# Performance work log

Measured on AMD Instinct MI355X. Metric: run time of the kernel, lower is better.

The kernel has to match this reference:

```python
import jax, jax.numpy as jnp
import numpy as np

HID = 10


def _lstm_cell(xt, h, c, W_ih, W_hh, b_ih, b_hh):
    # PyTorch LSTMCell: gates ordered (i, f, g, o)
    gates = xt @ W_ih.T + b_ih + h @ W_hh.T + b_hh  # [B, 4*HID]
    i, f, g, o = jnp.split(gates, 4, axis=-1)
    c_new = jax.nn.sigmoid(f) * c + jax.nn.sigmoid(i) * jnp.tanh(g)
    h_new = jax.nn.sigmoid(o) * jnp.tanh(c_new)
    return h_new, c_new


def setup_inputs() -> dict:
    key = jax.random.key(0)
    ks = jax.random.split(key, 12)
    B, T = 2048, 1024
    s = 0.1
    return {
        "x": jax.random.normal(ks[0], (B, T), dtype=jnp.float32),
        "W_ih1": jax.random.normal(ks[1], (4 * HID, 1), dtype=jnp.float32) * s,
        "W_hh1": jax.random.normal(ks[2], (4 * HID, HID), dtype=jnp.float32) * s,
        "b_ih1": jax.random.normal(ks[3], (4 * HID,), dtype=jnp.float32) * s,
        "b_hh1": jax.random.normal(ks[4], (4 * HID,), dtype=jnp.float32) * s,
        "W_ih2": jax.random.normal(ks[5], (4 * HID, HID), dtype=jnp.float32) * s,
        "W_hh2": jax.random.normal(ks[6], (4 * HID, HID), dtype=jnp.float32) * s,
        "b_ih2": jax.random.normal(ks[7], (4 * HID,), dtype=jnp.float32) * s,
        "b_ih2b": None,  # placeholder removed below
        "b_hh2": jax.random.normal(ks[8], (4 * HID,), dtype=jnp.float32) * s,
        "W_lin": jax.random.normal(ks[9], (1, HID), dtype=jnp.float32) * s,
        "b_lin": jax.random.normal(ks[10], (1,), dtype=jnp.float32) * s,
        "future": 64,
    } if False else {
        "x": jax.random.normal(ks[0], (B, T), dtype=jnp.float32),
        "W_ih1": jax.random.normal(ks[1], (4 * HID, 1), dtype=jnp.float32) * s,
        "W_hh1": jax.random.normal(ks[2], (4 * HID, HID), dtype=jnp.float32) * s,
        "b_ih1": jax.random.normal(ks[3], (4 * HID,), dtype=jnp.float32) * s,
        "b_hh1": jax.random.normal(ks[4], (4 * HID,), dtype=jnp.float32) * s,
        "W_ih2": jax.random.normal(ks[5], (4 * HID, HID), dtype=jnp.float32) * s,
        "W_hh2": jax.random.normal(ks[6], (4 * HID, HID), dtype=jnp.float32) * s,
        "b_ih2": jax.random.normal(ks[7], (4 * HID,), dtype=jnp.float32) * s,
        "b_hh2": jax.random.normal(ks[8], (4 * HID,), dtype=jnp.float32) * s,
        "W_lin": jax.random.normal(ks[9], (1, HID), dtype=jnp.float32) * s,
        "b_lin": jax.random.normal(ks[10], (1,), dtype=jnp.float32) * s,
        "future": 64,
    }


def _forward(x, W_ih1, W_hh1, b_ih1, b_hh1, W_ih2, W_hh2, b_ih2, b_hh2,
             W_lin, b_lin, future):
    B = x.shape[0]
    z = jnp.zeros((B, HID), dtype=x.dtype)
    state0 = (z, z, z, z)  # h1, c1, h2, c2

    def step(state, xt):
        h1, c1, h2, c2 = state
        h1, c1 = _lstm_cell(xt, h1, c1, W_ih1, W_hh1, b_ih1, b_hh1)
        h2, c2 = _lstm_cell(h1, h2, c2, W_ih2, W_hh2, b_ih2, b_hh2)
        y = h2 @ W_lin.T + b_lin  # [B, 1]
        return (h1, c1, h2, c2), y

    xs = x.T[:, :, None]  # [T, B, 1]
    state, ys = jax.lax.scan(step, state0, xs)  # ys: [T, B, 1]
    outs = ys[:, :, 0].T  # [B, T]

    if future > 0:
        last = ys[-1]  # [B, 1]

        def fstep(carry, _):
            state, y = carry
            state, y_new = step(state, y)
            return (state, y_new), y_new

        (_, _), fys = jax.lax.scan(fstep, (state, last), None, length=future)
        outs = jnp.concatenate([outs, fys[:, :, 0].T], axis=1)
    return outs  # [B, T + future]


def reference(x, W_ih1, W_hh1, b_ih1, b_hh1, W_ih2, W_hh2, b_ih2, b_hh2,
              W_lin, b_lin, future):
    return _forward(x, W_ih1, W_hh1, b_ih1, b_hh1, W_ih2, W_hh2, b_ih2,
                    b_hh2, W_lin, b_lin, future)
```

## Files before the change

kernel.cpp:

```cpp
#include <hip/hip_runtime.h>


#define NB 1024
#define TMAIN 1024
#define HID 10

typedef float v2f __attribute__((ext_vector_type(2)));

#define PIN2(v) asm volatile("" : "+v"(v))
#define PIN(v)  asm volatile("" : "+v"(v))

__device__ __forceinline__ float rcp_(float v)  { return __builtin_amdgcn_rcpf(v); }
__device__ __forceinline__ float exp2_(float v) { return __builtin_amdgcn_exp2f(v); }
__device__ __forceinline__ v2f mk2(float x, float y) { v2f r; r.x = x; r.y = y; return r; }
__device__ __forceinline__ v2f pfma(v2f a, v2f b, v2f c) { return __builtin_elementwise_fma(a, b, c); }

template<int J>
__device__ __forceinline__ float bc32(float v) {
    return __int_as_float(__builtin_amdgcn_ds_swizzle(__float_as_int(v), (J << 5)));
}
__device__ __forceinline__ float swz16(float v) {
    return __int_as_float(__builtin_amdgcn_ds_swizzle(__float_as_int(v), 0x401F));
}
__device__ __forceinline__ void bcast10(float h, float* hb) {
    hb[0] = bc32<0>(h); hb[1] = bc32<1>(h); hb[2] = bc32<2>(h); hb[3] = bc32<3>(h);
    hb[4] = bc32<4>(h); hb[5] = bc32<5>(h); hb[6] = bc32<6>(h); hb[7] = bc32<7>(h);
    hb[8] = bc32<8>(h); hb[9] = bc32<9>(h);
}

__global__ __launch_bounds__(64)
__attribute__((amdgpu_waves_per_eu(1)))
void lstm2_kernel(
    const float* __restrict__ x,
    const float* __restrict__ Wih1, const float* __restrict__ Whh1,
    const float* __restrict__ bih1, const float* __restrict__ bhh1,
    const float* __restrict__ Wih2, const float* __restrict__ Whh2,
    const float* __restrict__ bih2, const float* __restrict__ bhh2,
    const float* __restrict__ Wlin, const float* __restrict__ blin,
    const int* __restrict__ futp,
    float* __restrict__ out)
{
    const int lane = threadIdx.x;
    const int e    = lane >> 5;
    const int r1   = (lane >> 4) & 1;
    const int u    = lane & 15;
    const int ge   = blockIdx.x * 2 + e;
    const int F    = futp[0];
    const int OUTW = TMAIN + F;

    const bool uok = (u < HID);
    const int  uu  = uok ? u : 0;
    const int  Llo = (r1 ? 2 : 0) * HID + uu;
    const int  Lhi = (r1 ? 3 : 1) * HID + uu;

    const float tK   = 2.8853900817779268f;
    const float sK   = -1.4426950408889634f;
    const float aKlo = r1 ? tK : sK;
    const float aKhi = sK;
    const v2f aA2 = r1 ? mk2(tK, 0.f)       : mk2(0.f, 0.f);
    const v2f aB2 = r1 ? mk2(-2.f*tK, 1.f)  : mk2(1.f, 1.f);

    const float mu = uok ? 1.f : 0.f;
    v2f whh1p[10], wih2p[10], whh2p[10];
    float wl[10];
    #pragma unroll
    for (int j = 0; j < HID; ++j) {
        whh1p[j] = mk2(mu * aKlo * Whh1[Llo*HID + j], mu * aKhi * Whh1[Lhi*HID + j]);
        wih2p[j] = mk2(mu * aKlo * Wih2[Llo*HID + j], mu * aKhi * Wih2[Lhi*HID + j]);
        whh2p[j] = mk2(mu * aKlo * Whh2[Llo*HID + j], mu * aKhi * Whh2[Lhi*HID + j]);
        wl[j]    = Wlin[j];
    }
    v2f b1pk   = mk2(mu * aKlo * (bih1[Llo] + bhh1[Llo]),
                     mu * aKhi * (bih1[Lhi] + bhh1[Lhi]));
    v2f b2pk   = mk2(mu * aKlo * (bih2[Llo] + bhh2[Llo]),
                     mu * aKhi * (bih2[Lhi] + bhh2[Lhi]));
    v2f wih1pk = mk2(mu * aKlo * Wih1[Llo], mu * aKhi * Wih1[Lhi]);
    float bl = blin[0];

    #pragma unroll
    for (int j = 0; j < HID; ++j) { PIN2(whh1p[j]); PIN2(wih2p[j]); PIN2(whh2p[j]); PIN(wl[j]); }
    PIN2(b1pk); PIN2(b2pk); PIN2(wih1pk); PIN(bl);

    auto actf2 = [&](v2f p) -> v2f {
        v2f q;
        q.x = rcp_(1.0f + exp2_(p.x));
        q.y = rcp_(1.0f + exp2_(p.y));
        return pfma(aB2, q, aA2);
    };
    auto ctanh_ = [&](float cs) -> float {
        return fmaf(-2.0f, rcp_(1.0f + exp2_(cs)), 1.0f);
    };

    float c1 = 0.f, c2 = 0.f;
    float h1b[10], h2b[10];
    #pragma unroll
    for (int j = 0; j < HID; ++j) { h1b[j] = 0.f; h2b[j] = 0.f; }

    auto gates = [&](v2f a, float& gi, float& gf, float& gg, float& go) {
        float ox = swz16(a.x);
        float oy = swz16(a.y);
        gi = r1 ? ox  : a.x;
        gf = r1 ? oy  : a.y;
        gg = r1 ? a.x : ox;
        go = r1 ? a.y : oy;
    };
    auto dot10p = [&](const v2f* w, const float* hb, v2f init) -> v2f {
        v2f P = pfma(w[0], mk2(hb[0], hb[0]), init);
        v2f Q = w[1] * mk2(hb[1], hb[1]);
        #pragma unroll
        for (int j = 2; j < HID; j += 2) {
            P = pfma(w[j],     mk2(hb[j],     hb[j]),     P);
            Q = pfma(w[j + 1], mk2(hb[j + 1], hb[j + 1]), Q);
        }
        return P + Q;
    };
    auto head_ = [&]() -> float {
        float Y = fmaf(wl[0], h2b[0], bl);
        float Z = wl[1] * h2b[1];
        #pragma unroll
        for (int j = 2; j < HID; j += 2) {
            Y = fmaf(wl[j],     h2b[j],     Y);
            Z = fmaf(wl[j + 1], h2b[j + 1], Z);
        }
        return Y + Z;
    };

    auto cell2head = [&]() -> float {
        v2f U = dot10p(wih2p, h1b, b2pk);
        v2f V = dot10p(whh2p, h2b, mk2(0.f, 0.f));
        v2f a2 = actf2(U + V);
        float i2, f2, g2, o2; gates(a2, i2, f2, g2, o2);
        c2 = fmaf(f2, c2, i2 * g2);
        float h2n = o2 * ctanh_(c2);
        bcast10(h2n, h2b);
        return head_();
    };

    auto pipe_iter = [&](float xn) -> float {
        v2f U = dot10p(wih2p, h1b, b2pk);
        v2f V = dot10p(whh2p, h2b, mk2(0.f, 0.f));
        v2f A = dot10p(whh1p, h1b, pfma(wih1pk, mk2(xn, xn), b1pk));
        v2f a2 = actf2(U + V);
        v2f a1 = actf2(A);
        float i2, f2, g2, o2; gates(a2, i2, f2, g2, o2);
        float i1, f1, g1, o1; gates(a1, i1, f1, g1, o1);
        c2 = fmaf(f2, c2, i2 * g2);
        c1 = fmaf(f1, c1, i1 * g1);
        float h2n = o2 * ctanh_(c2);
        float h1n = o1 * ctanh_(c1);
        bcast10(h2n, h2b);
        bcast10(h1n, h1b);
        return head_();
    };

    auto fstep = [&](float yt) -> float {
        v2f A = dot10p(whh1p, h1b, pfma(wih1pk, mk2(yt, yt), b1pk));
        v2f a1 = actf2(A);
        float i1, f1, g1, o1; gates(a1, i1, f1, g1, o1);
        c1 = fmaf(f1, c1, i1 * g1);
        float h1n = o1 * ctanh_(c1);
        bcast10(h1n, h1b);
        return cell2head();
    };

    const float4* xrow = (const float4*)(x + (size_t)ge * TMAIN);
    float4* orow = (float4*)(out + (size_t)ge * OUTW);
    float4 xv = xrow[0];
    {
        v2f a1 = actf2(pfma(wih1pk, mk2(xv.x, xv.x), b1pk));
        float i1, f1, g1, o1; gates(a1, i1, f1, g1, o1);
        c1 = i1 * g1;
        float h1n = o1 * ctanh_(c1);
        bcast10(h1n, h1b);
    }

    #pragma unroll 1
    for (int t4 = 0; t4 < TMAIN / 4 - 1; ++t4) {
        float4 xn = xrow[t4 + 1];
        float y0 = pipe_iter(xv.y);
        float y1 = pipe_iter(xv.z);
        float y2 = pipe_iter(xv.w);
        float y3 = pipe_iter(xn.x);
        if ((lane & 31) == 0) orow[t4] = make_float4(y0, y1, y2, y3);
        xv = xn;
    }
    {
        float y0 = pipe_iter(xv.y);
        float y1 = pipe_iter(xv.z);
        float y2 = pipe_iter(xv.w);
        float y3 = cell2head();
        if ((lane & 31) == 0) orow[TMAIN / 4 - 1] = make_float4(y0, y1, y2, y3);
    }

    float yprev = head_();
    int t = 0;
    #pragma unroll 1
    for (; t + 3 < F; t += 4) {
        float y0 = fstep(yprev);
        float y1 = fstep(y0);
        float y2 = fstep(y1);
        float y3 = fstep(y2);
        if ((lane & 31) == 0) orow[(TMAIN + t) / 4] = make_float4(y0, y1, y2, y3);
        yprev = y3;
    }
    #pragma unroll 1
    for (; t < F; ++t) {
        yprev = fstep(yprev);
        if ((lane & 31) == 0) out[(size_t)ge * OUTW + TMAIN + t] = yprev;
    }
}

extern "C" void kernel_launch(void* const* d_in, const int* in_sizes, int n_in,
                              void* d_out, int out_size, void* d_ws, size_t ws_size,
                              hipStream_t stream) {
    const float* x    = (const float*)d_in[0];
    const float* Wih1 = (const float*)d_in[1];
    const float* Whh1 = (const float*)d_in[2];
    const float* bih1 = (const float*)d_in[3];
    const float* bhh1 = (const float*)d_in[4];
    const float* Wih2 = (const float*)d_in[5];
    const float* Whh2 = (const float*)d_in[6];
    const float* bih2 = (const float*)d_in[7];
    const float* bhh2 = (const float*)d_in[8];
    const float* Wlin = (const float*)d_in[9];
    const float* blin = (const float*)d_in[10];
    const int*   futp = (const int*)d_in[11];
    float* out = (float*)d_out;

    lstm2_kernel<<<NB, 64, 0, stream>>>(x, Wih1, Whh1, bih1, bhh1,
                                        Wih2, Whh2, bih2, bhh2,
                                        Wlin, blin, futp, out);
}
```

Measured before the change: 395.4 us.

## Map each sequence to 16 lanes holding all four gates per hidden unit

Each 16-lane group now computes all four gates of one hidden unit with 4-wide vector FMAs. Previously each sequence used 32 lanes split over gate pairs, and a swizzle exchanged gates between the halves. The change removes the cross-half gate exchange and the select logic, and packs four sequences per wave, which halves the block count. The trade is more ALU and transcendental work per lane for each step, which lengthens the serial per-step dependency chain, while half as many waves run.

```diff
diff --git a/kernel.cpp b/kernel.cpp
--- a/kernel.cpp
+++ b/kernel.cpp
@@ -1,31 +1,31 @@
 #include <hip/hip_runtime.h>
 
 
-#define NB 1024
+#define NB 512
 #define TMAIN 1024
 #define HID 10
 
-typedef float v2f __attribute__((ext_vector_type(2)));
-
-#define PIN2(v) asm volatile("" : "+v"(v))
+typedef float v4f __attribute__((ext_vector_type(4)));
+
+#define PIN4(v) asm volatile("" : "+v"(v))
 #define PIN(v)  asm volatile("" : "+v"(v))
 
 __device__ __forceinline__ float rcp_(float v)  { return __builtin_amdgcn_rcpf(v); }
 __device__ __forceinline__ float exp2_(float v) { return __builtin_amdgcn_exp2f(v); }
-__device__ __forceinline__ v2f mk2(float x, float y) { v2f r; r.x = x; r.y = y; return r; }
-__device__ __forceinline__ v2f pfma(v2f a, v2f b, v2f c) { return __builtin_elementwise_fma(a, b, c); }
+__device__ __forceinline__ v4f mk4(float a, float b, float c, float d) {
+    v4f r; r.x = a; r.y = b; r.z = c; r.w = d; return r;
+}
+__device__ __forceinline__ v4f splat4(float s) { return mk4(s, s, s, s); }
+__device__ __forceinline__ v4f pfma4(v4f a, v4f b, v4f c) { return __builtin_elementwise_fma(a, b, c); }
 
 template<int J>
-__device__ __forceinline__ float bc32(float v) {
-    return __int_as_float(__builtin_amdgcn_ds_swizzle(__float_as_int(v), (J << 5)));
-}
-__device__ __forceinline__ float swz16(float v) {
-    return __int_as_float(__builtin_amdgcn_ds_swizzle(__float_as_int(v), 0x401F));
+__device__ __forceinline__ float bc16(float v) {
+    return __int_as_float(__builtin_amdgcn_ds_swizzle(__float_as_int(v), (J << 5) | 0x10));
 }
 __device__ __forceinline__ void bcast10(float h, float* hb) {
-    hb[0] = bc32<0>(h); hb[1] = bc32<1>(h); hb[2] = bc32<2>(h); hb[3] = bc32<3>(h);
-    hb[4] = bc32<4>(h); hb[5] = bc32<5>(h); hb[6] = bc32<6>(h); hb[7] = bc32<7>(h);
-    hb[8] = bc32<8>(h); hb[9] = bc32<9>(h);
+    hb[0] = bc16<0>(h); hb[1] = bc16<1>(h); hb[2] = bc16<2>(h); hb[3] = bc16<3>(h);
+    hb[4] = bc16<4>(h); hb[5] = bc16<5>(h); hb[6] = bc16<6>(h); hb[7] = bc16<7>(h);
+    hb[8] = bc16<8>(h); hb[9] = bc16<9>(h);
 }
 
 __global__ __launch_bounds__(64)
@@ -41,54 +41,64 @@
     float* __restrict__ out)
 {
     const int lane = threadIdx.x;
-    const int e    = lane >> 5;
-    const int r1   = (lane >> 4) & 1;
+    const int e    = lane >> 4;
     const int u    = lane & 15;
-    const int ge   = blockIdx.x * 2 + e;
+    const int ge   = blockIdx.x * 4 + e;
     const int F    = futp[0];
     const int OUTW = TMAIN + F;
 
     const bool uok = (u < HID);
     const int  uu  = uok ? u : 0;
-    const int  Llo = (r1 ? 2 : 0) * HID + uu;
-    const int  Lhi = (r1 ? 3 : 1) * HID + uu;
-
-    const float tK   = 2.8853900817779268f;
-    const float sK   = -1.4426950408889634f;
-    const float aKlo = r1 ? tK : sK;
-    const float aKhi = sK;
-    const v2f aA2 = r1 ? mk2(tK, 0.f)       : mk2(0.f, 0.f);
-    const v2f aB2 = r1 ? mk2(-2.f*tK, 1.f)  : mk2(1.f, 1.f);
-
+    const int  Ri  = 0 * HID + uu;
+    const int  Rf  = 1 * HID + uu;
+    const int  Rg  = 2 * HID + uu;
+    const int  Ro  = 3 * HID + uu;
+
+    const float tK = 2.8853900817779268f;
+    const float sK = -1.4426950408889634f;
     const float mu = uok ? 1.f : 0.f;
-    v2f whh1p[10], wih2p[10], whh2p[10];
+    const v4f aK4 = mk4(mu * sK, mu * sK, mu * tK, mu * sK);
+    const v4f aA4 = mk4(0.f, 0.f, tK, 0.f);
+    const v4f aB4 = mk4(1.f, 1.f, -2.f * tK, 1.f);
+
+    v4f whh1q[10], wih2q[10], whh2q[10];
     float wl[10];
     #pragma unroll
     for (int j = 0; j < HID; ++j) {
-        whh1p[j] = mk2(mu * aKlo * Whh1[Llo*HID + j], mu * aKhi * Whh1[Lhi*HID + j]);
-        wih2p[j] = mk2(mu * aKlo * Wih2[Llo*HID + j], mu * aKhi * Wih2[Lhi*HID + j]);
-        whh2p[j] = mk2(mu * aKlo * Whh2[Llo*HID + j], mu * aKhi * Whh2[Lhi*HID + j]);
+        whh1q[j] = aK4 * mk4(Whh1[Ri*HID + j], Whh1[Rf*HID + j],
+                             Whh1[Rg*HID + j], Whh1[Ro*HID + j]);
+        wih2q[j] = aK4 * mk4(Wih2[Ri*HID + j], Wih2[Rf*HID + j],
+                             Wih2[Rg*HID + j], Wih2[Ro*HID + j]);
+        whh2q[j] = aK4 * mk4(Whh2[Ri*HID + j], Whh2[Rf*HID + j],
+                             Whh2[Rg*HID + j], Whh2[Ro*HID + j]);
         wl[j]    = Wlin[j];
     }
-    v2f b1pk   = mk2(mu * aKlo * (bih1[Llo] + bhh1[Llo]),
-                     mu * aKhi * (bih1[Lhi] + bhh1[Lhi]));
-    v2f b2pk   = mk2(mu * aKlo * (bih2[Llo] + bhh2[Llo]),
-                     mu * aKhi * (bih2[Lhi] + bhh2[Lhi]));
-    v2f wih1pk = mk2(mu * aKlo * Wih1[Llo], mu * aKhi * Wih1[Lhi]);
+    v4f b1q   = aK4 * mk4(bih1[Ri] + bhh1[Ri], bih1[Rf] + bhh1[Rf],
+                          bih1[Rg] + bhh1[Rg], bih1[Ro] + bhh1[Ro]);
+    v4f b2q   = aK4 * mk4(bih2[Ri] + bhh2[Ri], bih2[Rf] + bhh2[Rf],
+                          bih2[Rg] + bhh2[Rg], bih2[Ro] + bhh2[Ro]);
+    v4f wih1q = aK4 * mk4(Wih1[Ri], Wih1[Rf], Wih1[Rg], Wih1[Ro]);
     float bl = blin[0];
 
     #pragma unroll
-    for (int j = 0; j < HID; ++j) { PIN2(whh1p[j]); PIN2(wih2p[j]); PIN2(whh2p[j]); PIN(wl[j]); }
-    PIN2(b1pk); PIN2(b2pk); PIN2(wih1pk); PIN(bl);
-
-    auto actf2 = [&](v2f p) -> v2f {
-        v2f q;
+    for (int j = 0; j < HID; ++j) { PIN4(whh1q[j]); PIN4(wih2q[j]); PIN4(whh2q[j]); PIN(wl[j]); }
+    PIN4(b1q); PIN4(b2q); PIN4(wih1q); PIN(bl);
+
+    auto act4 = [&](v4f p) -> v4f {
+        v4f q;
         q.x = rcp_(1.0f + exp2_(p.x));
         q.y = rcp_(1.0f + exp2_(p.y));
-        return pfma(aB2, q, aA2);
+        q.z = rcp_(1.0f + exp2_(p.z));
+        q.w = rcp_(1.0f + exp2_(p.w));
+        return pfma4(aB4, q, aA4);
     };
     auto ctanh_ = [&](float cs) -> float {
         return fmaf(-2.0f, rcp_(1.0f + exp2_(cs)), 1.0f);
+    };
+    auto cellup = [&](v4f pre, float& c) -> float {
+        v4f a = act4(pre);
+        c = fmaf(a.y, c, a.x * a.z);
+        return a.w * ctanh_(c);
     };
 
     float c1 = 0.f, c2 = 0.f;
@@ -96,21 +106,13 @@
     #pragma unroll
     for (int j = 0; j < HID; ++j) { h1b[j] = 0.f; h2b[j] = 0.f; }
 
-    auto gates = [&](v2f a, float& gi, float& gf, float& gg, float& go) {
-        float ox = swz16(a.x);
-        float oy = swz16(a.y);
-        gi = r1 ? ox  : a.x;
-        gf = r1 ? oy  : a.y;
-        gg = r1 ? a.x : ox;
-        go = r1 ? a.y : oy;
-    };
-    auto dot10p = [&](const v2f* w, const float* hb, v2f init) -> v2f {
-        v2f P = pfma(w[0], mk2(hb[0], hb[0]), init);
-        v2f Q = w[1] * mk2(hb[1], hb[1]);
+    auto dot10q = [&](const v4f* w, const float* hb, v4f init) -> v4f {
+        v4f P = pfma4(w[0], splat4(hb[0]), init);
+        v4f Q = w[1] * splat4(hb[1]);
         #pragma unroll
         for (int j = 2; j < HID; j += 2) {
-            P = pfma(w[j],     mk2(hb[j],     hb[j]),     P);
-            Q = pfma(w[j + 1], mk2(hb[j + 1], hb[j + 1]), Q);
+            P = pfma4(w[j],     splat4(hb[j]),     P);
+            Q = pfma4(w[j + 1], splat4(hb[j + 1]), Q);
         }
         return P + Q;
     };
@@ -126,39 +128,27 @@
     };
 
     auto cell2head = [&]() -> float {
-        v2f U = dot10p(wih2p, h1b, b2pk);
-        v2f V = dot10p(whh2p, h2b, mk2(0.f, 0.f));
-        v2f a2 = actf2(U + V);
-        float i2, f2, g2, o2; gates(a2, i2, f2, g2, o2);
-        c2 = fmaf(f2, c2, i2 * g2);
-        float h2n = o2 * ctanh_(c2);
+        v4f U = dot10q(wih2q, h1b, b2q);
+        v4f V = dot10q(whh2q, h2b, splat4(0.f));
+        float h2n = cellup(U + V, c2);
         bcast10(h2n, h2b);
         return head_();
     };
 
     auto pipe_iter = [&](float xn) -> float {
-        v2f U = dot10p(wih2p, h1b, b2pk);
-        v2f V = dot10p(whh2p, h2b, mk2(0.f, 0.f));
-        v2f A = dot10p(whh1p, h1b, pfma(wih1pk, mk2(xn, xn), b1pk));
-        v2f a2 = actf2(U + V);
-        v2f a1 = actf2(A);
-        float i2, f2, g2, o2; gates(a2, i2, f2, g2, o2);
-        float i1, f1, g1, o1; gates(a1, i1, f1, g1, o1);
-        c2 = fmaf(f2, c2, i2 * g2);
-        c1 = fmaf(f1, c1, i1 * g1);
-        float h2n = o2 * ctanh_(c2);
-        float h1n = o1 * ctanh_(c1);
+        v4f U = dot10q(wih2q, h1b, b2q);
+        v4f V = dot10q(whh2q, h2b, splat4(0.f));
+        v4f A = dot10q(whh1q, h1b, pfma4(wih1q, splat4(xn), b1q));
+        float h2n = cellup(U + V, c2);
+        float h1n = cellup(A, c1);
         bcast10(h2n, h2b);
         bcast10(h1n, h1b);
         return head_();
     };
 
     auto fstep = [&](float yt) -> float {
-        v2f A = dot10p(whh1p, h1b, pfma(wih1pk, mk2(yt, yt), b1pk));
-        v2f a1 = actf2(A);
-        float i1, f1, g1, o1; gates(a1, i1, f1, g1, o1);
-        c1 = fmaf(f1, c1, i1 * g1);
-        float h1n = o1 * ctanh_(c1);
+        v4f A = dot10q(whh1q, h1b, pfma4(wih1q, splat4(yt), b1q));
+        float h1n = cellup(A, c1);
         bcast10(h1n, h1b);
         return cell2head();
     };
@@ -167,10 +157,9 @@
     float4* orow = (float4*)(out + (size_t)ge * OUTW);
     float4 xv = xrow[0];
     {
-        v2f a1 = actf2(pfma(wih1pk, mk2(xv.x, xv.x), b1pk));
-        float i1, f1, g1, o1; gates(a1, i1, f1, g1, o1);
-        c1 = i1 * g1;
-        float h1n = o1 * ctanh_(c1);
+        v4f a1 = act4(pfma4(wih1q, splat4(xv.x), b1q));
+        c1 = a1.x * a1.z;
+        float h1n = a1.w * ctanh_(c1);
         bcast10(h1n, h1b);
     }
 
@@ -181,7 +170,7 @@
         float y1 = pipe_iter(xv.z);
         float y2 = pipe_iter(xv.w);
         float y3 = pipe_iter(xn.x);
-        if ((lane & 31) == 0) orow[t4] = make_float4(y0, y1, y2, y3);
+        if (u == 0) orow[t4] = make_float4(y0, y1, y2, y3);
         xv = xn;
     }
     {
@@ -189,7 +178,7 @@
         float y1 = pipe_iter(xv.z);
         float y2 = pipe_iter(xv.w);
         float y3 = cell2head();
-        if ((lane & 31) == 0) orow[TMAIN / 4 - 1] = make_float4(y0, y1, y2, y3);
+        if (u == 0) orow[TMAIN / 4 - 1] = make_float4(y0, y1, y2, y3);
     }
 
     float yprev = head_();
@@ -200,13 +189,13 @@
         float y1 = fstep(y0);
         float y2 = fstep(y1);
         float y3 = fstep(y2);
-        if ((lane & 31) == 0) orow[(TMAIN + t) / 4] = make_float4(y0, y1, y2, y3);
+        if (u == 0) orow[(TMAIN + t) / 4] = make_float4(y0, y1, y2, y3);
         yprev = y3;
     }
     #pragma unroll 1
     for (; t < F; ++t) {
         yprev = fstep(yprev);
-        if ((lane & 31) == 0) out[(size_t)ge * OUTW + TMAIN + t] = yprev;
+        if (u == 0) out[(size_t)ge * OUTW + TMAIN + t] = yprev;
     }
 }
 
```

After: 459.9 us. +16.3%, slower.
